# Optimization experiments

Measured on AMD Instinct MI355X. Metric: run time of the kernel, lower is better.

The kernel has to match this reference:

```python
import jax, jax.numpy as jnp
import numpy as np

OUTPUT_DIM = 512
INPUT_DIM = 64
BATCH = 131072


def setup_inputs() -> dict:
    key = jax.random.key(0)
    k1, k2, k3, k4 = jax.random.split(key, 4)
    D = INPUT_DIM + OUTPUT_DIM
    X = jax.random.normal(k1, (BATCH, OUTPUT_DIM), dtype=jnp.float32)
    c = jax.random.normal(k2, (BATCH, INPUT_DIM), dtype=jnp.float32)
    PA = jax.random.normal(k3, (OUTPUT_DIM, D), dtype=jnp.float32) * 0.05
    PB = jax.random.normal(k4, (OUTPUT_DIM, D), dtype=jnp.float32) * 0.05
    return {"X": X, "c": c, "PA": PA, "PB": PB}


def reference(X, c, PA, PB):
    # x = cat(c, X) : [B, D] with D = INPUT_DIM + OUTPUT_DIM
    x = jnp.concatenate([c, X], axis=1)
    D = INPUT_DIM + OUTPUT_DIM
    mask = (jnp.arange(D)[None, :] < (INPUT_DIM + jnp.arange(OUTPUT_DIM))[:, None]).astype(x.dtype)
    A = x @ (PA * mask).T  # [B, OUTPUT_DIM], A[:, i] = pa[i] @ x[:, :INPUT_DIM+i]
    Bv = x @ (PB * mask).T  # [B, OUTPUT_DIM]
    z = X * jnp.exp(A) + Bv  # [B, OUTPUT_DIM]
    log_det = jnp.sum(A, axis=1)  # [B]
    return z, log_det
```

## Files before the change

kernel.cpp:

```cpp
#include <hip/hip_runtime.h>
#include <stdint.h>

#define N_OUT 512
#define N_IN 64
#define D_TOT 576
#define BM 64
#define ROW_BYTES (D_TOT * 2)

typedef __attribute__((ext_vector_type(8))) short short8_t;
typedef __attribute__((ext_vector_type(4))) float f32x4;
typedef unsigned short u16;

__device__ __forceinline__ u16 f2bf(float f) {
    union { float f; uint32_t u; } v;
    v.f = f;
    uint32_t r = v.u + 0x7FFFu + ((v.u >> 16) & 1u);
    return (u16)(r >> 16);
}
__device__ __forceinline__ float bf2f(u16 u) {
    union { uint32_t u; float f; } v;
    v.u = ((uint32_t)u) << 16;
    return v.f;
}

__global__ void prep_weights_kernel(const float* __restrict__ PA,
                                    const float* __restrict__ PB,
                                    u16* __restrict__ WA,
                                    u16* __restrict__ WB) {
    const int row = blockIdx.x;
    const int lim = N_IN + row;
    const float* pa = PA + (size_t)row * D_TOT;
    const float* pb = PB + (size_t)row * D_TOT;
    u16* wa = WA + (size_t)row * D_TOT;
    u16* wb = WB + (size_t)row * D_TOT;
    for (int j = threadIdx.x; j < D_TOT; j += blockDim.x) {
        bool valid = (j < lim);
        wa[j] = valid ? f2bf(pa[j]) : (u16)0;
        wb[j] = valid ? f2bf(pb[j]) : (u16)0;
    }
}

__global__ __launch_bounds__(256, 2)
void maf_main_kernel(const float* __restrict__ X,
                     const float* __restrict__ Cc,
                     const u16* __restrict__ WA,
                     const u16* __restrict__ WB,
                     float* __restrict__ Z,
                     float* __restrict__ LD) {
    extern __shared__ char smem[];
    char* xt = smem;
    float* ldsum = (float*)(smem + BM * ROW_BYTES);

    const int tid = threadIdx.x;
    const int r0 = blockIdx.x * BM;

    #pragma unroll
    for (int i = 0; i < 2; ++i) {
        int id = tid + i * 256;
        int row = id >> 3, cc = id & 7;
        const float* src = Cc + (size_t)(r0 + row) * N_IN + cc * 8;
        f32x4 v0 = *(const f32x4*)src;
        f32x4 v1 = *(const f32x4*)(src + 4);
        short8_t p;
        p[0] = (short)f2bf(v0[0]); p[1] = (short)f2bf(v0[1]);
        p[2] = (short)f2bf(v0[2]); p[3] = (short)f2bf(v0[3]);
        p[4] = (short)f2bf(v1[0]); p[5] = (short)f2bf(v1[1]);
        p[6] = (short)f2bf(v1[2]); p[7] = (short)f2bf(v1[3]);
        int addr = (row * ROW_BYTES + cc * 16) ^ ((row & 7) << 4);
        *(short8_t*)(xt + addr) = p;
    }
    #pragma unroll
    for (int i = 0; i < 16; ++i) {
        int id = tid + i * 256;
        int row = id >> 6, xc = id & 63;
        const float* src = X + (size_t)(r0 + row) * N_OUT + xc * 8;
        f32x4 v0 = *(const f32x4*)src;
        f32x4 v1 = *(const f32x4*)(src + 4);
        short8_t p;
        p[0] = (short)f2bf(v0[0]); p[1] = (short)f2bf(v0[1]);
        p[2] = (short)f2bf(v0[2]); p[3] = (short)f2bf(v0[3]);
        p[4] = (short)f2bf(v1[0]); p[5] = (short)f2bf(v1[1]);
        p[6] = (short)f2bf(v1[2]); p[7] = (short)f2bf(v1[3]);
        int addr = (row * ROW_BYTES + (8 + xc) * 16) ^ ((row & 7) << 4);
        *(short8_t*)(xt + addr) = p;
    }
    __syncthreads();

    const int wid = tid >> 6;
    const int lane = tid & 63;
    const int lr = lane & 15;
    const int lg = lane >> 4;

    float part[4][4];
    #pragma unroll
    for (int m = 0; m < 4; ++m)
        #pragma unroll
        for (int j = 0; j < 4; ++j) part[m][j] = 0.0f;

    const int groups[4] = { wid, 7 - wid, 8 + wid, 15 - wid };

    #pragma unroll
    for (int gi = 0; gi < 4; ++gi) {
        const int g = groups[gi];
        const int c0 = g << 5;
        const int ksteps = 3 + g;

        f32x4 accA[4][2], accB[4][2];
        #pragma unroll
        for (int m = 0; m < 4; ++m)
            #pragma unroll
            for (int n = 0; n < 2; ++n) {
                accA[m][n] = (f32x4)(0.0f);
                accB[m][n] = (f32x4)(0.0f);
            }

        #pragma unroll 2
        for (int kk = 0; kk < ksteps; ++kk) {
            const int kb = kk * 64 + lg * 16;
            short8_t a[4];
            #pragma unroll
            for (int m = 0; m < 4; ++m) {
                int row = (m << 4) + lr;
                int addr = (row * ROW_BYTES + kb) ^ ((row & 7) << 4);
                a[m] = *(const short8_t*)(xt + addr);
            }
            short8_t ba[2], bb[2];
            #pragma unroll
            for (int n = 0; n < 2; ++n) {
                int col = c0 + (n << 4) + lr;
                size_t off = (size_t)col * D_TOT + (size_t)(kk * 32 + lg * 8);
                ba[n] = *(const short8_t*)(WA + off);
                bb[n] = *(const short8_t*)(WB + off);
            }
            #pragma unroll
            for (int m = 0; m < 4; ++m) {
                #pragma unroll
                for (int n = 0; n < 2; ++n) {
                    accA[m][n] = __builtin_amdgcn_mfma_f32_16x16x32_bf16(a[m], ba[n], accA[m][n], 0, 0, 0);
                    accB[m][n] = __builtin_amdgcn_mfma_f32_16x16x32_bf16(a[m], bb[n], accB[m][n], 0, 0, 0);
                }
            }
        }

        #pragma unroll
        for (int m = 0; m < 4; ++m) {
            #pragma unroll
            for (int n = 0; n < 2; ++n) {
                int col = c0 + (n << 4) + lr;
                #pragma unroll
                for (int j = 0; j < 4; ++j) {
                    int row = (m << 4) + (lg << 2) + j;
                    float Av = accA[m][n][j];
                    float Bv = accB[m][n][j];
                    int xaddr = (row * ROW_BYTES + (N_IN + col) * 2) ^ ((row & 7) << 4);
                    float Xf = bf2f(*(const u16*)(xt + xaddr));
                    Z[(size_t)(r0 + row) * N_OUT + col] = Xf * __expf(Av) + Bv;
                    part[m][j] += Av;
                }
            }
        }
    }

    #pragma unroll
    for (int m = 0; m < 4; ++m) {
        #pragma unroll
        for (int j = 0; j < 4; ++j) {
            float v = part[m][j];
            v += __shfl_xor(v, 1);
            v += __shfl_xor(v, 2);
            v += __shfl_xor(v, 4);
            v += __shfl_xor(v, 8);
            if (lr == 0) ldsum[(wid << 6) + (m << 4) + (lg << 2) + j] = v;
        }
    }
    __syncthreads();
    if (tid < 64) {
        float s = ldsum[tid] + ldsum[64 + tid] + ldsum[128 + tid] + ldsum[192 + tid];
        LD[(size_t)r0 + tid] = s;
    }
}

extern "C" void kernel_launch(void* const* d_in, const int* in_sizes, int n_in,
                              void* d_out, int out_size, void* d_ws, size_t ws_size,
                              hipStream_t stream) {
    const float* X  = (const float*)d_in[0];
    const float* Cc = (const float*)d_in[1];
    const float* PA = (const float*)d_in[2];
    const float* PB = (const float*)d_in[3];

    u16* WA = (u16*)d_ws;
    u16* WB = WA + (size_t)N_OUT * D_TOT;

    float* Z  = (float*)d_out;
    const size_t batch = (size_t)in_sizes[0] / N_OUT;
    float* LD = Z + batch * N_OUT;

    prep_weights_kernel<<<N_OUT, 256, 0, stream>>>(PA, PB, WA, WB);

    const size_t lds_bytes = (size_t)BM * ROW_BYTES + 4 * 64 * sizeof(float);
    (void)hipFuncSetAttribute((const void*)maf_main_kernel,
                              hipFuncAttributeMaxDynamicSharedMemorySize,
                              (int)lds_bytes);
    const int grid = (int)(batch / BM);
    maf_main_kernel<<<grid, 256, lds_bytes, stream>>>(X, Cc, WA, WB, Z, LD);
}
```

Measured before the change: 246.2 us.

## Use 8-wave blocks and pre-swizzle bf16 weights for coalesced fragment loads

Raises the block size from 256 to 512 threads, so each of eight waves handles two balanced column groups instead of four. The weight-prep kernel now stores the bf16 weights in an MFMA-fragment-major layout, so lanes in a wave read contiguous 16-byte chunks rather than rows strided by D_TOT. It also swaps the handwritten float-to-bf16 rounding for the HIP intrinsic and unrolls the k-loop by three. The aim is more in-flight waves per CU and better-coalesced weight traffic. The cost is higher LDS and register pressure per block, and launch_bounds(512,4) may force register spills.

```diff
diff --git a/kernel.cpp b/kernel.cpp
--- a/kernel.cpp
+++ b/kernel.cpp
@@ -1,4 +1,5 @@
 #include <hip/hip_runtime.h>
+#include <hip/hip_bf16.h>
 #include <stdint.h>
 
 #define N_OUT 512
@@ -6,16 +7,15 @@
 #define D_TOT 576
 #define BM 64
 #define ROW_BYTES (D_TOT * 2)
+#define NWAVES 8
 
 typedef __attribute__((ext_vector_type(8))) short short8_t;
 typedef __attribute__((ext_vector_type(4))) float f32x4;
 typedef unsigned short u16;
 
 __device__ __forceinline__ u16 f2bf(float f) {
-    union { float f; uint32_t u; } v;
-    v.f = f;
-    uint32_t r = v.u + 0x7FFFu + ((v.u >> 16) & 1u);
-    return (u16)(r >> 16);
+    __hip_bfloat16 h = __float2bfloat16(f);
+    return *reinterpret_cast<u16*>(&h);
 }
 __device__ __forceinline__ float bf2f(u16 u) {
     union { uint32_t u; float f; } v;
@@ -27,20 +27,20 @@
                                     const float* __restrict__ PB,
                                     u16* __restrict__ WA,
                                     u16* __restrict__ WB) {
-    const int row = blockIdx.x;
-    const int lim = N_IN + row;
-    const float* pa = PA + (size_t)row * D_TOT;
-    const float* pb = PB + (size_t)row * D_TOT;
-    u16* wa = WA + (size_t)row * D_TOT;
-    u16* wb = WB + (size_t)row * D_TOT;
-    for (int j = threadIdx.x; j < D_TOT; j += blockDim.x) {
-        bool valid = (j < lim);
-        wa[j] = valid ? f2bf(pa[j]) : (u16)0;
-        wb[j] = valid ? f2bf(pb[j]) : (u16)0;
-    }
-}
-
-__global__ __launch_bounds__(256, 2)
+    const int col = blockIdx.x;
+    const int lim = N_IN + col;
+    const float* pa = PA + (size_t)col * D_TOT;
+    const float* pb = PB + (size_t)col * D_TOT;
+    for (int k = threadIdx.x; k < D_TOT; k += blockDim.x) {
+        int kk = k >> 5, lg = (k >> 3) & 3, j = k & 7;
+        size_t dst = ((size_t)(kk * 4 + lg) * N_OUT + col) * 8 + j;
+        bool valid = (k < lim);
+        WA[dst] = valid ? f2bf(pa[k]) : (u16)0;
+        WB[dst] = valid ? f2bf(pb[k]) : (u16)0;
+    }
+}
+
+__global__ __launch_bounds__(512, 4)
 void maf_main_kernel(const float* __restrict__ X,
                      const float* __restrict__ Cc,
                      const u16* __restrict__ WA,
@@ -54,10 +54,8 @@
     const int tid = threadIdx.x;
     const int r0 = blockIdx.x * BM;
 
-    #pragma unroll
-    for (int i = 0; i < 2; ++i) {
-        int id = tid + i * 256;
-        int row = id >> 3, cc = id & 7;
+    {
+        int row = tid >> 3, cc = tid & 7;
         const float* src = Cc + (size_t)(r0 + row) * N_IN + cc * 8;
         f32x4 v0 = *(const f32x4*)src;
         f32x4 v1 = *(const f32x4*)(src + 4);
@@ -70,8 +68,8 @@
         *(short8_t*)(xt + addr) = p;
     }
     #pragma unroll
-    for (int i = 0; i < 16; ++i) {
-        int id = tid + i * 256;
+    for (int i = 0; i < 8; ++i) {
+        int id = tid + i * 512;
         int row = id >> 6, xc = id & 63;
         const float* src = X + (size_t)(r0 + row) * N_OUT + xc * 8;
         f32x4 v0 = *(const f32x4*)src;
@@ -97,10 +95,10 @@
         #pragma unroll
         for (int j = 0; j < 4; ++j) part[m][j] = 0.0f;
 
-    const int groups[4] = { wid, 7 - wid, 8 + wid, 15 - wid };
-
-    #pragma unroll
-    for (int gi = 0; gi < 4; ++gi) {
+    const int groups[2] = { wid, 15 - wid };
+
+    #pragma unroll
+    for (int gi = 0; gi < 2; ++gi) {
         const int g = groups[gi];
         const int c0 = g << 5;
         const int ksteps = 3 + g;
@@ -114,7 +112,7 @@
                 accB[m][n] = (f32x4)(0.0f);
             }
 
-        #pragma unroll 2
+        #pragma unroll 3
         for (int kk = 0; kk < ksteps; ++kk) {
             const int kb = kk * 64 + lg * 16;
             short8_t a[4];
@@ -125,10 +123,10 @@
                 a[m] = *(const short8_t*)(xt + addr);
             }
             short8_t ba[2], bb[2];
+            const size_t wbase = (size_t)((kk << 2) + lg) * N_OUT + c0 + lr;
             #pragma unroll
             for (int n = 0; n < 2; ++n) {
-                int col = c0 + (n << 4) + lr;
-                size_t off = (size_t)col * D_TOT + (size_t)(kk * 32 + lg * 8);
+                size_t off = (wbase + (n << 4)) * 8;
                 ba[n] = *(const short8_t*)(WA + off);
                 bb[n] = *(const short8_t*)(WB + off);
             }
@@ -175,7 +173,9 @@
     }
     __syncthreads();
     if (tid < 64) {
-        float s = ldsum[tid] + ldsum[64 + tid] + ldsum[128 + tid] + ldsum[192 + tid];
+        float s = 0.0f;
+        #pragma unroll
+        for (int w = 0; w < NWAVES; ++w) s += ldsum[(w << 6) + tid];
         LD[(size_t)r0 + tid] = s;
     }
 }
@@ -197,10 +197,10 @@
 
     prep_weights_kernel<<<N_OUT, 256, 0, stream>>>(PA, PB, WA, WB);
 
-    const size_t lds_bytes = (size_t)BM * ROW_BYTES + 4 * 64 * sizeof(float);
+    const size_t lds_bytes = (size_t)BM * ROW_BYTES + NWAVES * 64 * sizeof(float);
     (void)hipFuncSetAttribute((const void*)maf_main_kernel,
                               hipFuncAttributeMaxDynamicSharedMemorySize,
                               (int)lds_bytes);
     const int grid = (int)(batch / BM);
-    maf_main_kernel<<<grid, 256, lds_bytes, stream>>>(X, Cc, WA, WB, Z, LD);
-}
+    maf_main_kernel<<<grid, 512, lds_bytes, stream>>>(X, Cc, WA, WB, Z, LD);
+}
```

New measurement: 248.9 us. No clear change (+1.1%).
